# Kernel tuning notes

Measured on AMD Instinct MI355X. Metric: run time of the kernel, lower is better.

## Reference

```python
import jax, jax.numpy as jnp
import numpy as np
import math

B, L, IN, HID, NLAYERS, AA = 16, 512, 512, 512, 6, 21
KAPPA_ADD = 5.0


def _sru_layer(x, W, v, b):
    # x: [L, B, din]; W: [din, 2*HID*k]; v, b: [2(gate f/r), 2(dir), HID]
    Lx, Bx, din = x.shape
    d = HID
    k = W.shape[1] // (2 * d)  # 4 if projecting residual, 3 if residual = input
    U = (x @ W).reshape(Lx, Bx, 2, d, k)
    res = U[..., 3] if k == 4 else x.reshape(Lx, Bx, 2, d)
    # time-flip direction 1 so a single scan handles both directions
    flip = lambda a: jnp.concatenate([a[:, :, :1], a[::-1, :, 1:]], axis=2)
    u0, u1, u2, resf = flip(U[..., 0]), flip(U[..., 1]), flip(U[..., 2]), flip(res)
    vf, vr = v[0], v[1]
    bf, br = b[0], b[1]

    def step(c, t):
        u0t, u1t, u2t, rt = t
        f = jax.nn.sigmoid(u1t + vf * c + bf)
        c1 = f * c + (1.0 - f) * u0t
        r = jax.nn.sigmoid(u2t + vr * c1 + br)
        h = r * c1 + (1.0 - r) * rt
        return c1, h

    c0 = jnp.zeros((Bx, 2, d), x.dtype)
    _, H = jax.lax.scan(step, c0, (u0, u1, u2, resf))
    return flip(H).reshape(Lx, Bx, 2 * d)


def setup_inputs():
    key = jax.random.key(0)
    inp = {}
    inp['input'] = jax.random.normal(jax.random.fold_in(key, 0), (B, L, IN), jnp.float32)
    inp['hidden'] = jnp.zeros((NLAYERS, B, 2 * HID), jnp.float32)
    for l in range(NLAYERS):
        din = IN if l == 0 else 2 * HID
        k = 4 if din != 2 * HID else 3
        inp[f'sru_w{l}'] = jax.random.normal(jax.random.fold_in(key, 10 + l), (din, 2 * HID * k), jnp.float32) * (1.0 / math.sqrt(din))
        inp[f'sru_v{l}'] = jax.random.normal(jax.random.fold_in(key, 20 + l), (2, 2, HID), jnp.float32) * 0.1
        inp[f'sru_b{l}'] = jnp.zeros((2, 2, HID), jnp.float32)

    def lin(seed, din, dout):
        w = jax.random.normal(jax.random.fold_in(key, seed), (din, dout), jnp.float32) * (1.0 / math.sqrt(din))
        return w, jnp.zeros((dout,), jnp.float32)

    inp['fc1_logits_w'], inp['fc1_logits_b'] = lin(30, 2 * HID, HID)
    inp['fc2_logits_w'], inp['fc2_logits_b'] = lin(31, HID, AA)
    inp['fc1_angles_w'], inp['fc1_angles_b'] = lin(32, 2 * HID, HID)
    inp['fc2_means_w'], inp['fc2_means_b'] = lin(33, HID, 2)
    inp['fc2_kappas_w'], inp['fc2_kappas_b'] = lin(34, HID, 2)
    return inp


def reference(input, hidden, sru_w0, sru_v0, sru_b0, sru_w1, sru_v1, sru_b1, sru_w2, sru_v2, sru_b2, sru_w3, sru_v3, sru_b3, sru_w4, sru_v4, sru_b4, sru_w5, sru_v5, sru_b5, fc1_logits_w, fc1_logits_b, fc2_logits_w, fc2_logits_b, fc1_angles_w, fc1_angles_b, fc2_means_w, fc2_means_b, fc2_kappas_w, fc2_kappas_b):
    x = input.transpose(1, 0, 2)  # [L, B, IN]
    ws = [sru_w0, sru_w1, sru_w2, sru_w3, sru_w4, sru_w5]
    vs = [sru_v0, sru_v1, sru_v2, sru_v3, sru_v4, sru_v5]
    bs = [sru_b0, sru_b1, sru_b2, sru_b3, sru_b4, sru_b5]
    for W, v, b in zip(ws, vs, bs):
        x = _sru_layer(x, W, v, b)
    sru_out = x.transpose(1, 0, 2)  # [B, L, 2*HID]
    h_log = sru_out @ fc1_logits_w + fc1_logits_b
    output_logits = jax.nn.log_softmax(h_log @ fc2_logits_w + fc2_logits_b, axis=-1)
    h_ang = sru_out @ fc1_angles_w + fc1_angles_b
    output_means = jnp.tanh(h_ang @ fc2_means_w + fc2_means_b) * math.pi
    output_kappas = KAPPA_ADD + jax.nn.softplus(h_ang @ fc2_kappas_w + fc2_kappas_b)
    return (output_logits, output_means, output_kappas)
```

## Files before the change

kernel.cpp:

```cpp
#include <hip/hip_runtime.h>

typedef __attribute__((ext_vector_type(8))) short short8;
typedef __attribute__((ext_vector_type(4))) float f32x4;

__device__ __forceinline__ ushort f2bf(float x) {
  unsigned u = __builtin_bit_cast(unsigned, x);
  u = (u + 0x7fffu + ((u >> 16) & 1u)) >> 16;
  return (ushort)u;
}
__device__ __forceinline__ float bf2f(ushort x) {
  return __builtin_bit_cast(float, ((unsigned)x) << 16);
}

#define AS1CP(p) ((const __attribute__((address_space(1))) unsigned int*)(p))
#define AS3CP(p) ((__attribute__((address_space(3))) unsigned int*)(p))
#define GLDS(g, l, SZ) __builtin_amdgcn_global_load_lds(AS1CP(g), AS3CP(l), SZ, 0, 0)

__global__ __launch_bounds__(256) void k_cvt(const float* __restrict__ in,
                                             ushort* __restrict__ out, int n4) {
  int i = blockIdx.x * 256 + threadIdx.x;
  if (i >= n4) return;
  float4 v = reinterpret_cast<const float4*>(in)[i];
  ushort4 o;
  o.x = f2bf(v.x); o.y = f2bf(v.y); o.z = f2bf(v.z); o.w = f2bf(v.w);
  reinterpret_cast<ushort4*>(out)[i] = o;
}

__global__ __launch_bounds__(256) void k_transpose(const float* __restrict__ W,
                                                   ushort* __restrict__ Wt,
                                                   int N, int K) {
  __shared__ float tile[32][33];
  int bx = blockIdx.x * 32;
  int by = blockIdx.y * 32;
  int tx = threadIdx.x, ty = threadIdx.y;
#pragma unroll
  for (int i = 0; i < 32; i += 8)
    tile[ty + i][tx] = W[(size_t)(by + ty + i) * N + bx + tx];
  __syncthreads();
#pragma unroll
  for (int i = 0; i < 32; i += 8)
    Wt[(size_t)(bx + ty + i) * K + by + tx] = f2bf(tile[tx][ty + i]);
}

template <int BF16OUT>
__global__ __launch_bounds__(256) void k_gemm(const ushort* __restrict__ A,
                                              const ushort* __restrict__ Bt,
                                              void* __restrict__ Cv,
                                              int K, int N) {
  __shared__ __align__(16) ushort lsA[2][4096];
  __shared__ __align__(16) ushort lsB[2][4096];
  const int tid = threadIdx.x;
  const int bm = blockIdx.x, bn = blockIdx.y;
  const int w = tid >> 6, l = tid & 63;
  const int wm = (w >> 1) * 64, wn = (w & 1) * 64;
  const int lr = l & 15, lg = l >> 4;
  f32x4 acc[4][4] = {};
  const int srow = tid >> 2;
  const int scol = (tid & 3) * 8;
  const ushort* Ag = A + (size_t)(bm * 128 + srow) * K + scol;
  const ushort* Bg = Bt + (size_t)(bn * 128 + srow) * K + scol;
  const int nt = K >> 5;

#define GEMM_ISSUE(BUF, KT)                                       \
  {                                                               \
    GLDS(Ag + (KT), &lsA[BUF][w * 512], 16);                      \
    GLDS(Ag + (size_t)64 * K + (KT), &lsA[BUF][2048 + w * 512], 16); \
    GLDS(Bg + (KT), &lsB[BUF][w * 512], 16);                      \
    GLDS(Bg + (size_t)64 * K + (KT), &lsB[BUF][2048 + w * 512], 16); \
  }

  GEMM_ISSUE(0, 0);
  for (int t = 0; t < nt; ++t) {
    const int cur = t & 1;
    if (t + 1 < nt) {
      GEMM_ISSUE(cur ^ 1, (t + 1) * 32);
      asm volatile("s_waitcnt vmcnt(4)" ::: "memory");
    } else {
      asm volatile("s_waitcnt vmcnt(0)" ::: "memory");
    }
    asm volatile("s_barrier" ::: "memory");
    short8 af[4], bfr[4];
#pragma unroll
    for (int i = 0; i < 4; ++i)
      af[i] = *(const short8*)&lsA[cur][(wm + i * 16 + lr) * 32 + lg * 8];
#pragma unroll
    for (int j = 0; j < 4; ++j)
      bfr[j] = *(const short8*)&lsB[cur][(wn + j * 16 + lr) * 32 + lg * 8];
#pragma unroll
    for (int i = 0; i < 4; ++i)
#pragma unroll
      for (int j = 0; j < 4; ++j)
        acc[i][j] = __builtin_amdgcn_mfma_f32_16x16x32_bf16(af[i], bfr[j], acc[i][j], 0, 0, 0);
    asm volatile("s_barrier" ::: "memory");
  }
#undef GEMM_ISSUE
  const size_t cbase = (size_t)(bm * 128 + wm + lg * 4) * N + bn * 128 + wn + lr;
  if (BF16OUT) {
    ushort* Cb = (ushort*)Cv + cbase;
#pragma unroll
    for (int i = 0; i < 4; ++i)
#pragma unroll
      for (int j = 0; j < 4; ++j)
#pragma unroll
        for (int r = 0; r < 4; ++r)
          Cb[(size_t)(i * 16 + r) * N + j * 16] = f2bf(acc[i][j][r]);
  } else {
    float* Cb = (float*)Cv + cbase;
#pragma unroll
    for (int i = 0; i < 4; ++i)
#pragma unroll
      for (int j = 0; j < 4; ++j)
#pragma unroll
        for (int r = 0; r < 4; ++r)
          Cb[(size_t)(i * 16 + r) * N + j * 16] = acc[i][j][r];
  }
}

template <int KK>
__device__ __forceinline__ void tile_wait3(int i) {
  if (KK == 3) {
    if (i <= 29)
      asm volatile("s_waitcnt vmcnt(63)" ::: "memory");
    else if (i == 30)
      asm volatile("s_waitcnt vmcnt(32)" ::: "memory");
    else
      asm volatile("s_waitcnt vmcnt(0)" ::: "memory");
  } else {
    if (i <= 29)
      asm volatile("s_waitcnt vmcnt(32)" ::: "memory");
    else if (i == 30)
      asm volatile("s_waitcnt vmcnt(16)" ::: "memory");
    else
      asm volatile("s_waitcnt vmcnt(0)" ::: "memory");
  }
}

template <int KK>
__global__ __launch_bounds__(64, 1) void sru_rec4(const float* __restrict__ U,
                                                  const ushort* __restrict__ Xres,
                                                  const float* __restrict__ v,
                                                  const float* __restrict__ bb,
                                                  ushort* __restrict__ H) {
  const int lane = threadIdx.x;
  if (lane >= 16) return;
  const int blk = blockIdx.x;
  const int b = blk >> 6, rem = blk & 63, dir = rem >> 5, c0 = (rem & 31) << 4;
  const int h = c0 + lane;
  const float vf = v[dir * 512 + h], vr = v[1024 + dir * 512 + h];
  const float bfv = bb[dir * 512 + h], brv = bb[1024 + dir * 512 + h];
  const int rs = 1024 * KK;
  const int tstep = dir ? -1 : 1;
  const int t0 = dir ? 511 : 0;
  const float* Ub = U + (size_t)b * 512 * rs + dir * 512 * KK + (size_t)h * KK;
  const ushort* Xb = Xres + (size_t)b * 512 * 1024 + dir * 512 + h;
  ushort* Hb = H + (size_t)b * 512 * 1024 + dir * 512 + h;

  float4 u4[4][16];
  float3 u3[4][16];
  ushort xr[4][16];

#define SR_ISSUE(J, TI)                                                        \
  {                                                                            \
    const int base_ = (TI) * 16;                                               \
    _Pragma("unroll")                                                          \
    for (int t = 0; t < 16; ++t) {                                             \
      int tt = t0 + tstep * (base_ + t);                                       \
      if (KK == 4) {                                                           \
        u4[J][t] = *(const float4*)(Ub + (size_t)tt * rs);                     \
      } else {                                                                 \
        u3[J][t] = *(const float3*)(Ub + (size_t)tt * rs);                     \
        xr[J][t] = Xb[(size_t)tt * 1024];                                      \
      }                                                                        \
    }                                                                          \
  }

#define SR_COMP(J, TI)                                                         \
  {                                                                            \
    _Pragma("unroll")                                                          \
    for (int s = 0; s < 16; ++s) {                                             \
      float u0, u1, u2, uR;                                                    \
      if (KK == 4) {                                                           \
        u0 = u4[J][s].x; u1 = u4[J][s].y; u2 = u4[J][s].z; uR = u4[J][s].w;    \
      } else {                                                                 \
        u0 = u3[J][s].x; u1 = u3[J][s].y; u2 = u3[J][s].z; uR = bf2f(xr[J][s]);\
      }                                                                        \
      float f = __builtin_amdgcn_rcpf(1.f + __expf(-(u1 + vf * c + bfv)));     \
      c = u0 + f * (c - u0);                                                   \
      float r = __builtin_amdgcn_rcpf(1.f + __expf(-(u2 + vr * c + brv)));     \
      float hh = uR + r * (c - uR);                                            \
      Hb[(size_t)(t0 + tstep * ((TI) * 16 + s)) * 1024] = f2bf(hh);            \
    }                                                                          \
  }

  SR_ISSUE(0, 0)
  SR_ISSUE(1, 1)
  SR_ISSUE(2, 2)

  float c = 0.f;
#pragma unroll 1
  for (int ii = 0; ii < 8; ++ii) {
#define TILE_J(J)                                                              \
    {                                                                          \
      const int i = ii * 4 + (J);                                              \
      tile_wait3<KK>(i);                                                       \
      SR_COMP(J, i)                                                            \
      if (i + 3 < 32) SR_ISSUE((((J) + 3) & 3), i + 3)                         \
    }
    TILE_J(0) TILE_J(1) TILE_J(2) TILE_J(3)
#undef TILE_J
  }
#undef SR_ISSUE
#undef SR_COMP
}

__global__ __launch_bounds__(256) void k_buildW2(const float* __restrict__ w2l,
                                                 const float* __restrict__ w2m,
                                                 const float* __restrict__ w2k,
                                                 ushort* __restrict__ Wt2) {
  int i = blockIdx.x * 256 + threadIdx.x;
  if (i >= 128 * 1024) return;
  int n = i >> 10, k = i & 1023;
  float vv = 0.f;
  if (n < 21 && k < 512) vv = w2l[k * 21 + n];
  else if (n >= 21 && n < 23 && k >= 512) vv = w2m[(k - 512) * 2 + (n - 21)];
  else if (n >= 23 && n < 25 && k >= 512) vv = w2k[(k - 512) * 2 + (n - 23)];
  Wt2[i] = f2bf(vv);
}

__global__ __launch_bounds__(64) void k_bias25(const float* __restrict__ b1l,
                                               const float* __restrict__ b1a,
                                               const float* __restrict__ w2l,
                                               const float* __restrict__ b2l,
                                               const float* __restrict__ w2m,
                                               const float* __restrict__ b2m,
                                               const float* __restrict__ w2k,
                                               const float* __restrict__ b2k,
                                               float* __restrict__ b2adj) {
  int o = threadIdx.x;
  if (o >= 25) return;
  float s;
  if (o < 21) {
    s = b2l[o];
    for (int k = 0; k < 512; ++k) s += b1l[k] * w2l[k * 21 + o];
  } else if (o < 23) {
    s = b2m[o - 21];
    for (int k = 0; k < 512; ++k) s += b1a[k] * w2m[k * 2 + (o - 21)];
  } else {
    s = b2k[o - 23];
    for (int k = 0; k < 512; ++k) s += b1a[k] * w2k[k * 2 + (o - 23)];
  }
  b2adj[o] = s;
}

__global__ __launch_bounds__(64) void k_act(const float* __restrict__ T,
                                            const float* __restrict__ b2adj,
                                            float* __restrict__ out) {
  const int row = blockIdx.x;
  const int lane = threadIdx.x;
  float myv = 0.f;
  if (lane < 25) myv = T[(size_t)row * 128 + lane] + b2adj[lane];
  float x = (lane < 21) ? myv : -1e30f;
#pragma unroll
  for (int off = 32; off; off >>= 1) x = fmaxf(x, __shfl_xor(x, off));
  float e = (lane < 21) ? expf(myv - x) : 0.f;
#pragma unroll
  for (int off = 32; off; off >>= 1) e += __shfl_xor(e, off);
  float lse = x + logf(e);
  if (lane < 21) {
    out[(size_t)row * 21 + lane] = myv - lse;
  } else if (lane < 23) {
    out[172032 + row * 2 + (lane - 21)] = tanhf(myv) * 3.14159265358979323846f;
  } else if (lane < 25) {
    float sp = (myv > 20.f) ? myv : log1pf(expf(myv));
    out[188416 + row * 2 + (lane - 23)] = 5.f + sp;
  }
}

extern "C" void kernel_launch(void* const* d_in, const int* in_sizes, int n_in,
                              void* d_out, int out_size, void* d_ws, size_t ws_size,
                              hipStream_t stream) {
  (void)in_sizes; (void)n_in; (void)out_size; (void)ws_size;
  const float* input = (const float*)d_in[0];
  const float* sw[6]; const float* sv[6]; const float* sb[6];
  for (int l = 0; l < 6; ++l) {
    sw[l] = (const float*)d_in[2 + 3 * l];
    sv[l] = (const float*)d_in[3 + 3 * l];
    sb[l] = (const float*)d_in[4 + 3 * l];
  }
  const float* fc1lw = (const float*)d_in[20];
  const float* fc1lb = (const float*)d_in[21];
  const float* fc2lw = (const float*)d_in[22];
  const float* fc2lb = (const float*)d_in[23];
  const float* fc1aw = (const float*)d_in[24];
  const float* fc1ab = (const float*)d_in[25];
  const float* fc2mw = (const float*)d_in[26];
  const float* fc2mb = (const float*)d_in[27];
  const float* fc2kw = (const float*)d_in[28];
  const float* fc2kb = (const float*)d_in[29];

  char* ws = (char*)d_ws;
  float* U = (float*)ws;
  ushort* Hcat2 = (ushort*)ws;
  float* T = (float*)(ws + 67108864);
  ushort* H0 = (ushort*)(ws + 134217728);
  ushort* H1 = (ushort*)(ws + 150994944);
  ushort* X0 = (ushort*)(ws + 167772160);
  const size_t wbase = 176160768;
  ushort* Wtl[6];
  Wtl[0] = (ushort*)(ws + wbase);
  for (int l = 1; l < 6; ++l)
    Wtl[l] = (ushort*)(ws + wbase + 4194304 + (size_t)(l - 1) * 6291456);
  ushort* Wfc = (ushort*)(ws + wbase + 4194304 + 5ull * 6291456);
  ushort* Wt2 = (ushort*)(ws + wbase + 37748736);
  float* b2adj = (float*)(ws + wbase + 38010880);

  k_cvt<<<4096, 256, 0, stream>>>(input, X0, 8192 * 512 / 4);
  k_buildW2<<<512, 256, 0, stream>>>(fc2lw, fc2mw, fc2kw, Wt2);
  k_bias25<<<1, 64, 0, stream>>>(fc1lb, fc1ab, fc2lw, fc2lb, fc2mw, fc2mb,
                                 fc2kw, fc2kb, b2adj);

  k_transpose<<<dim3(4096 / 32, 512 / 32), dim3(32, 8), 0, stream>>>(sw[0], Wtl[0], 4096, 512);
  for (int l = 1; l < 6; ++l)
    k_transpose<<<dim3(3072 / 32, 1024 / 32), dim3(32, 8), 0, stream>>>(sw[l], Wtl[l], 3072, 1024);
  k_transpose<<<dim3(512 / 32, 1024 / 32), dim3(32, 8), 0, stream>>>(fc1lw, Wfc, 512, 1024);
  k_transpose<<<dim3(512 / 32, 1024 / 32), dim3(32, 8), 0, stream>>>(fc1aw, Wfc + (size_t)512 * 1024, 512, 1024);

  for (int l = 0; l < 6; ++l) {
    const ushort* Ain = (l == 0) ? X0 : ((l & 1) ? H0 : H1);
    ushort* Hout = (l & 1) ? H1 : H0;
    int K = (l == 0) ? 512 : 1024;
    int N = (l == 0) ? 4096 : 3072;
    k_gemm<0><<<dim3(64, N / 128), 256, 0, stream>>>(Ain, Wtl[l], U, K, N);
    if (l == 0)
      sru_rec4<4><<<1024, 64, 0, stream>>>(U, X0 , sv[l], sb[l], Hout);
    else
      sru_rec4<3><<<1024, 64, 0, stream>>>(U, Ain, sv[l], sb[l], Hout);
  }

  k_gemm<1><<<dim3(64, 8), 256, 0, stream>>>(H1, Wfc, Hcat2, 1024, 1024);

  k_gemm<0><<<dim3(64, 1), 256, 0, stream>>>(Hcat2, Wt2, T, 1024, 128);

  k_act<<<8192, 64, 0, stream>>>(T, b2adj, (float*)d_out);
}
```

Measured before the change: 885.3 us.

## Swizzle GEMM LDS layout and restructure SRU recurrence prefetch pipeline

The GEMM now XOR-swizzles the LDS column chunk per row on both the global-to-LDS store and the fragment reads, to cut LDS bank conflicts on the MFMA operand loads. The SRU recurrence kernel moves from 16-step to 8-step tiles with 64 tiles. It issues the next prefetch before computing the current tile, under a fixed vmcnt wait, to keep more loads in flight while registers stay bounded. The gate math is also folded into fused multiply-adds with pre-negated constants. The risks are more waitcnt and issue overhead per step and a wrong vmcnt count if the compiler reorders loads.

```diff
diff --git a/kernel.cpp b/kernel.cpp
--- a/kernel.cpp
+++ b/kernel.cpp
@@ -56,10 +56,11 @@
   const int lr = l & 15, lg = l >> 4;
   f32x4 acc[4][4] = {};
   const int srow = tid >> 2;
-  const int scol = (tid & 3) * 8;
+  const int scol = (((tid & 3) ^ ((srow >> 1) & 3))) * 8;
   const ushort* Ag = A + (size_t)(bm * 128 + srow) * K + scol;
   const ushort* Bg = Bt + (size_t)(bn * 128 + srow) * K + scol;
   const int nt = K >> 5;
+  const int rxor = (lr >> 1) & 3;
 
 #define GEMM_ISSUE(BUF, KT)                                       \
   {                                                               \
@@ -82,10 +83,10 @@
     short8 af[4], bfr[4];
 #pragma unroll
     for (int i = 0; i < 4; ++i)
-      af[i] = *(const short8*)&lsA[cur][(wm + i * 16 + lr) * 32 + lg * 8];
+      af[i] = *(const short8*)&lsA[cur][(wm + i * 16 + lr) * 32 + ((lg ^ rxor) * 8)];
 #pragma unroll
     for (int j = 0; j < 4; ++j)
-      bfr[j] = *(const short8*)&lsB[cur][(wn + j * 16 + lr) * 32 + lg * 8];
+      bfr[j] = *(const short8*)&lsB[cur][(wn + j * 16 + lr) * 32 + ((lg ^ rxor) * 8)];
 #pragma unroll
     for (int i = 0; i < 4; ++i)
 #pragma unroll
@@ -117,26 +118,7 @@
 }
 
 template <int KK>
-__device__ __forceinline__ void tile_wait3(int i) {
-  if (KK == 3) {
-    if (i <= 29)
-      asm volatile("s_waitcnt vmcnt(63)" ::: "memory");
-    else if (i == 30)
-      asm volatile("s_waitcnt vmcnt(32)" ::: "memory");
-    else
-      asm volatile("s_waitcnt vmcnt(0)" ::: "memory");
-  } else {
-    if (i <= 29)
-      asm volatile("s_waitcnt vmcnt(32)" ::: "memory");
-    else if (i == 30)
-      asm volatile("s_waitcnt vmcnt(16)" ::: "memory");
-    else
-      asm volatile("s_waitcnt vmcnt(0)" ::: "memory");
-  }
-}
-
-template <int KK>
-__global__ __launch_bounds__(64, 1) void sru_rec4(const float* __restrict__ U,
+__global__ __launch_bounds__(64, 1) void sru_rec5(const float* __restrict__ U,
                                                   const ushort* __restrict__ Xres,
                                                   const float* __restrict__ v,
                                                   const float* __restrict__ bb,
@@ -148,6 +130,8 @@
   const int h = c0 + lane;
   const float vf = v[dir * 512 + h], vr = v[1024 + dir * 512 + h];
   const float bfv = bb[dir * 512 + h], brv = bb[1024 + dir * 512 + h];
+  const float vfn = -vf, vrn = -vr;
+  const float kf0 = -bfv, kr0 = -brv;
   const int rs = 1024 * KK;
   const int tstep = dir ? -1 : 1;
   const int t0 = dir ? 511 : 0;
@@ -155,20 +139,20 @@
   const ushort* Xb = Xres + (size_t)b * 512 * 1024 + dir * 512 + h;
   ushort* Hb = H + (size_t)b * 512 * 1024 + dir * 512 + h;
 
-  float4 u4[4][16];
-  float3 u3[4][16];
-  ushort xr[4][16];
+  float4 r4[4][8];
+  float3 r3[4][8];
+  ushort xr[4][8];
 
 #define SR_ISSUE(J, TI)                                                        \
   {                                                                            \
-    const int base_ = (TI) * 16;                                               \
+    const int base_ = (TI) * 8;                                                \
     _Pragma("unroll")                                                          \
-    for (int t = 0; t < 16; ++t) {                                             \
+    for (int t = 0; t < 8; ++t) {                                              \
       int tt = t0 + tstep * (base_ + t);                                       \
       if (KK == 4) {                                                           \
-        u4[J][t] = *(const float4*)(Ub + (size_t)tt * rs);                     \
+        r4[J][t] = *(const float4*)(Ub + (size_t)tt * rs);                     \
       } else {                                                                 \
-        u3[J][t] = *(const float3*)(Ub + (size_t)tt * rs);                     \
+        r3[J][t] = *(const float3*)(Ub + (size_t)tt * rs);                     \
         xr[J][t] = Xb[(size_t)tt * 1024];                                      \
       }                                                                        \
     }                                                                          \
@@ -177,19 +161,27 @@
 #define SR_COMP(J, TI)                                                         \
   {                                                                            \
     _Pragma("unroll")                                                          \
-    for (int s = 0; s < 16; ++s) {                                             \
+    for (int s = 0; s < 8; ++s) {                                              \
       float u0, u1, u2, uR;                                                    \
       if (KK == 4) {                                                           \
-        u0 = u4[J][s].x; u1 = u4[J][s].y; u2 = u4[J][s].z; uR = u4[J][s].w;    \
+        u0 = r4[J][s].x; u1 = r4[J][s].y; u2 = r4[J][s].z; uR = r4[J][s].w;    \
       } else {                                                                 \
-        u0 = u3[J][s].x; u1 = u3[J][s].y; u2 = u3[J][s].z; uR = bf2f(xr[J][s]);\
+        u0 = r3[J][s].x; u1 = r3[J][s].y; u2 = r3[J][s].z; uR = bf2f(xr[J][s]);\
       }                                                                        \
-      float f = __builtin_amdgcn_rcpf(1.f + __expf(-(u1 + vf * c + bfv)));     \
-      c = u0 + f * (c - u0);                                                   \
-      float r = __builtin_amdgcn_rcpf(1.f + __expf(-(u2 + vr * c + brv)));     \
-      float hh = uR + r * (c - uR);                                            \
-      Hb[(size_t)(t0 + tstep * ((TI) * 16 + s)) * 1024] = f2bf(hh);            \
+      float ef = __expf(__builtin_fmaf(vfn, c, kf0 - u1));                     \
+      float f = __builtin_amdgcn_rcpf(1.f + ef);                               \
+      c = __builtin_fmaf(f, c - u0, u0);                                       \
+      float er = __expf(__builtin_fmaf(vrn, c, kr0 - u2));                     \
+      float r = __builtin_amdgcn_rcpf(1.f + er);                               \
+      float hh = __builtin_fmaf(r, c - uR, uR);                                \
+      Hb[(size_t)(t0 + tstep * ((TI) * 8 + s)) * 1024] = f2bf(hh);             \
     }                                                                          \
+  }
+
+#define SR_WAIT                                                                \
+  {                                                                            \
+    if (KK == 3) asm volatile("s_waitcnt vmcnt(32)" ::: "memory");             \
+    else         asm volatile("s_waitcnt vmcnt(16)" ::: "memory");             \
   }
 
   SR_ISSUE(0, 0)
@@ -198,19 +190,25 @@
 
   float c = 0.f;
 #pragma unroll 1
-  for (int ii = 0; ii < 8; ++ii) {
+  for (int ii = 0; ii < 15; ++ii) {
 #define TILE_J(J)                                                              \
     {                                                                          \
       const int i = ii * 4 + (J);                                              \
-      tile_wait3<KK>(i);                                                       \
+      SR_WAIT                                                                  \
+      SR_ISSUE((((J) + 3) & 3), i + 3)                                         \
       SR_COMP(J, i)                                                            \
-      if (i + 3 < 32) SR_ISSUE((((J) + 3) & 3), i + 3)                         \
     }
     TILE_J(0) TILE_J(1) TILE_J(2) TILE_J(3)
 #undef TILE_J
   }
+  SR_WAIT SR_ISSUE(3, 63) SR_COMP(0, 60)
+  SR_WAIT SR_COMP(1, 61)
+  SR_WAIT SR_COMP(2, 62)
+  asm volatile("s_waitcnt vmcnt(0)" ::: "memory");
+  SR_COMP(3, 63)
 #undef SR_ISSUE
 #undef SR_COMP
+#undef SR_WAIT
 }
 
 __global__ __launch_bounds__(256) void k_buildW2(const float* __restrict__ w2l,
@@ -332,9 +330,9 @@
     int N = (l == 0) ? 4096 : 3072;
     k_gemm<0><<<dim3(64, N / 128), 256, 0, stream>>>(Ain, Wtl[l], U, K, N);
     if (l == 0)
-      sru_rec4<4><<<1024, 64, 0, stream>>>(U, X0 , sv[l], sb[l], Hout);
+      sru_rec5<4><<<1024, 64, 0, stream>>>(U, X0 , sv[l], sb[l], Hout);
     else
-      sru_rec4<3><<<1024, 64, 0, stream>>>(U, Ain, sv[l], sb[l], Hout);
+      sru_rec5<3><<<1024, 64, 0, stream>>>(U, Ain, sv[l], sb[l], Hout);
   }
 
   k_gemm<1><<<dim3(64, 8), 256, 0, stream>>>(H1, Wfc, Hcat2, 1024, 1024);
```

Result: faster. 808.5 us (-8.7%).
